# Kernel tuning notes

Measured on AMD Instinct MI355X. Metric: run time of the kernel, lower is better.

Reference implementation:

```python
import jax, jax.numpy as jnp
import numpy as np

ROT = 0.7071  # matches the literal used in DiagPool's affine theta
EPS = 1e-5    # GroupNorm default eps


def conv2d(x, w, pad):
    # x: (N,C,H,W), w: (O,I,kh,kw)
    return jax.lax.conv_general_dilated(
        x, w, window_strides=(1, 1), padding=[(pad, pad), (pad, pad)],
        dimension_numbers=("NCHW", "OIHW", "NCHW"))


def diag_pool(x):
    """Replicates F.affine_grid + F.grid_sample (align_corners=False, bilinear,
    zeros padding) with a 45-degree rotation, then mean over H (keepdim)."""
    N, C, H, W = x.shape
    dt = x.dtype
    xn = ((2.0 * jnp.arange(W, dtype=dt) + 1.0) / W - 1.0)  # normalized x coords
    yn = ((2.0 * jnp.arange(H, dtype=dt) + 1.0) / H - 1.0)  # normalized y coords
    Yn, Xn = jnp.meshgrid(yn, xn, indexing="ij")            # (H,W)
    xs = ROT * Xn - ROT * Yn   # theta row 0
    ys = ROT * Xn + ROT * Yn   # theta row 1
    # unnormalize (align_corners=False)
    xp = ((xs + 1.0) * W - 1.0) * 0.5
    yp = ((ys + 1.0) * H - 1.0) * 0.5
    x0 = jnp.floor(xp); y0 = jnp.floor(yp)
    x1 = x0 + 1.0;      y1 = y0 + 1.0
    wx1 = xp - x0; wx0 = 1.0 - wx1
    wy1 = yp - y0; wy0 = 1.0 - wy1

    def gather(yi, xi):
        valid = ((yi >= 0) & (yi < H) & (xi >= 0) & (xi < W)).astype(dt)
        yc = jnp.clip(yi, 0, H - 1).astype(jnp.int32)
        xc = jnp.clip(xi, 0, W - 1).astype(jnp.int32)
        return x[:, :, yc, xc] * valid  # (N,C,H,W)

    rot = (gather(y0, x0) * (wy0 * wx0) + gather(y0, x1) * (wy0 * wx1)
           + gather(y1, x0) * (wy1 * wx0) + gather(y1, x1) * (wy1 * wx1))
    return rot.mean(axis=2, keepdims=True)  # (N,C,1,W)


def group_norm_per_channel(x, g, b):
    # GroupNorm(cg, cg): each channel normalized over its own (H,W)
    mu = x.mean(axis=(2, 3), keepdims=True)
    var = x.var(axis=(2, 3), keepdims=True)
    xh = (x - mu) * jax.lax.rsqrt(var + EPS)
    return xh * g[None, :, None, None] + b[None, :, None, None]


def cross_axis_encode(gx, axis_fuse_w, gn_w, gn_b):
    N, cg, H, W = gx.shape
    x_h = gx.mean(axis=3, keepdims=True)                 # (N,cg,H,1)
    x_w = gx.mean(axis=2, keepdims=True)                 # (N,cg,1,W)
    x_d = diag_pool(gx)                                  # (N,cg,1,W)
    fused = jnp.concatenate(
        [x_h, x_w.transpose(0, 1, 3, 2), x_d.transpose(0, 1, 3, 2)], axis=2)  # (N,cg,H+2W,1)
    fused = conv2d(fused, axis_fuse_w, 0)
    x_h2 = fused[:, :, :H]          # (N,cg,H,1)
    x_w2 = fused[:, :, H:H + W]     # (N,cg,W,1)
    out = gx * jax.nn.sigmoid(x_h2) * jax.nn.sigmoid(x_w2.transpose(0, 1, 3, 2))
    return group_norm_per_channel(out, gn_w, gn_b)


def setup_inputs() -> dict:
    key = jax.random.key(0)
    B, C, H, W = 8, 256, 128, 128
    G = 32
    cg = C // G  # 8
    ks = jax.random.split(key, 10)
    s = 0.1
    return {
        "x": jax.random.normal(ks[0], (B, C, H, W), jnp.float32),
        "axis_fuse_w": jax.random.normal(ks[1], (cg, cg, 1, 1), jnp.float32) * s,
        "gn_w": jnp.ones((cg,), jnp.float32),
        "gn_b": jnp.zeros((cg,), jnp.float32),
        "conv1x1_w": jax.random.normal(ks[2], (cg, cg, 1, 1), jnp.float32) * s,
        "conv3x3_w": jax.random.normal(ks[3], (cg, cg, 3, 3), jnp.float32) * s,
        "conv5x5_w": jax.random.normal(ks[4], (cg, cg, 5, 5), jnp.float32) * s,
        "scale_w": jnp.ones((3,), jnp.float32),
        "ch_gate_w": jax.random.normal(ks[5], (cg, cg, 1, 1), jnp.float32) * s,
        "sp_gate_w": jax.random.normal(ks[6], (1, cg, 1, 1), jnp.float32) * s,
        "groups": 32,
    }


def reference(x, axis_fuse_w, gn_w, gn_b, conv1x1_w, conv3x3_w, conv5x5_w,
              scale_w, ch_gate_w, sp_gate_w, groups):
    B, C, H, W = x.shape
    cg = C // groups
    N = B * groups
    gx = x.reshape(N, cg, H, W)

    xa = cross_axis_encode(gx, axis_fuse_w, gn_w, gn_b)
    xa = conv2d(xa, conv1x1_w, 0)
    xb = conv2d(gx, conv3x3_w, 1)
    xc = conv2d(gx, conv5x5_w, 2)

    sw = jax.nn.softmax(scale_w)
    x1 = sw[0] * xa + sw[1] * xb + sw[2] * xc
    x2 = xb

    def ch_gate(t):
        return jax.nn.sigmoid(conv2d(t.mean(axis=(2, 3), keepdims=True), ch_gate_w, 0))

    def sp_gate(t):
        return jax.nn.sigmoid(conv2d(t, sp_gate_w, 0))

    x1 = x1 * ch_gate(x1) * sp_gate(x1)
    x2 = x2 * ch_gate(x2) * sp_gate(x2)

    x11 = jax.nn.softmax(x1.mean(axis=(2, 3)).reshape(N, 1, cg), axis=-1)  # (N,1,cg)
    x12 = x2.reshape(N, cg, H * W)
    x21 = jax.nn.softmax(x2.mean(axis=(2, 3)).reshape(N, 1, cg), axis=-1)
    x22 = x1.reshape(N, cg, H * W)
    weights = (x11 @ x12 + x21 @ x22).reshape(N, 1, H, W)
    return (gx * jax.nn.sigmoid(weights)).reshape(B, C, H, W)
```

## Files before the change

kernel.cpp:

```cpp
#include <hip/hip_runtime.h>
#include <math.h>

#define HH 128
#define WW 128
#define CG 8
#define NN 256
#define HWSZ (HH*WW)
#define GB (36*36*8)

typedef __bf16 bf16x8 __attribute__((ext_vector_type(8)));
typedef short short8v __attribute__((ext_vector_type(8)));
typedef float f32x4 __attribute__((ext_vector_type(4)));

__device__ __forceinline__ float sigmoidf_(float x){ return 1.0f/(1.0f+__expf(-x)); }

__device__ __forceinline__ unsigned short f2bf(float x){
  __bf16 h = (__bf16)x;
  return __builtin_bit_cast(unsigned short, h);
}
__device__ __forceinline__ float bf2f(unsigned short h){
  union { unsigned u; float f; } v; v.u = ((unsigned)h) << 16; return v.f;
}

__device__ __forceinline__ float wx1_(const float* w1, const float* w3, const float* w5,
                                      float sw0, float sw1, float sw2,
                                      int oc, int ic, int tap){
  if (tap < 25){
    int ky = tap/5, kx = tap - ky*5;
    float wv = sw2 * w5[oc*200 + ic*25 + tap];
    if (ky >= 1 && ky <= 3 && kx >= 1 && kx <= 3)
      wv = fmaf(sw1, w3[oc*72 + ic*9 + (ky-1)*3 + (kx-1)], wv);
    return wv;
  }
  if (tap == 25) return sw0 * w1[oc*CG + ic];
  return 0.f;
}
__device__ __forceinline__ float wx2_(const float* w3, int oc, int ic, int tap){
  if (tap < 25){
    int ky = tap/5, kx = tap - ky*5;
    if (ky >= 1 && ky <= 3 && kx >= 1 && kx <= 3)
      return w3[oc*72 + ic*9 + (ky-1)*3 + (kx-1)];
  }
  return 0.f;
}

__global__ void kWB(const float* __restrict__ w1, const float* __restrict__ w3,
                    const float* __restrict__ w5, const float* __restrict__ scw,
                    const float* __restrict__ spw,
                    unsigned short* __restrict__ BH, unsigned short* __restrict__ BL){
  int e = blockIdx.x*256 + threadIdx.x;
  float a = scw[0], b = scw[1], c = scw[2];
  float m = fmaxf(a, fmaxf(b, c));
  float e0 = __expf(a-m), e1 = __expf(b-m), e2 = __expf(c-m);
  float inv = 1.0f/(e0+e1+e2);
  float sw0 = e0*inv, sw1 = e1*inv, sw2 = e2*inv;
  if (e < 3584){
    int s = e >> 9, rem = e & 511, nn = rem >> 5, kk = rem & 31;
    int tap = s*4 + (kk >> 3), ic = kk & 7;
    float wv = (nn < 8) ? wx1_(w1,w3,w5,sw0,sw1,sw2,nn,ic,tap)
                        : wx2_(w3,nn-8,ic,tap);
    BH[e] = f2bf(wv);
  } else if (e < 5824){
    int e2 = e - 3584;
    int s = e2 / 320, rem = e2 - s*320, nn = rem >> 5, kk = rem & 31;
    int tap = s*4 + (kk >> 3), ic = kk & 7;
    float outv;
    if (nn < 8){
      float wv = wx1_(w1,w3,w5,sw0,sw1,sw2,nn,ic,tap);
      outv = wv - bf2f(f2bf(wv));
    } else {
      float sum = 0.f;
      #pragma unroll
      for (int oc = 0; oc < CG; ++oc){
        float wv = (nn == 8) ? wx1_(w1,w3,w5,sw0,sw1,sw2,oc,ic,tap)
                             : wx2_(w3,oc,ic,tap);
        sum = fmaf(spw[oc], wv, sum);
      }
      outv = sum;
    }
    BL[e2] = f2bf(outv);
  }
}

__global__ __launch_bounds__(256) void kA1(const float* __restrict__ gx,
                                           float* __restrict__ xh_ws,
                                           float* __restrict__ xw_ws){
  int b = blockIdx.x; int n = b >> 3; int c = b & 7;
  int tid = threadIdx.x;
  __shared__ float colpart[2][WW];
  const float* img = gx + (size_t)(n*CG+c)*HWSZ;
  int w = tid & 127, half = tid >> 7;
  float acc = 0.f;
  const float* p = img + half*64*WW + w;
  for (int h = 0; h < 64; ++h) acc += p[h*WW];
  colpart[half][w] = acc;
  int h2 = tid >> 1, wh = tid & 1;
  float racc = 0.f;
  const float* rp = img + h2*WW + wh*64;
  for (int j = 0; j < 64; ++j) racc += rp[j];
  racc += __shfl_xor(racc, 1);
  __syncthreads();
  if (tid < WW) xw_ws[(n*CG+c)*WW + tid] = (colpart[0][tid] + colpart[1][tid]) * (1.0f/HH);
  if (wh == 0) xh_ws[(n*CG+c)*HH + h2] = racc * (1.0f/WW);
}

__global__ __launch_bounds__(256) void kA2(const float* __restrict__ xh_ws,
                                           const float* __restrict__ xw_ws,
                                           const float* __restrict__ afw,
                                           float* __restrict__ sig_h,
                                           float* __restrict__ sig_w){
  int n = blockIdx.x;
  int tid = threadIdx.x;
  if (tid < HH){
    int h = tid;
    float v[CG];
    #pragma unroll
    for (int c = 0; c < CG; ++c) v[c] = xh_ws[(n*CG+c)*HH + h];
    #pragma unroll
    for (int o = 0; o < CG; ++o){
      float s = 0.f;
      #pragma unroll
      for (int i = 0; i < CG; ++i) s = fmaf(afw[o*CG+i], v[i], s);
      sig_h[(n*CG+o)*HH + h] = sigmoidf_(s);
    }
  } else {
    int w = tid - 128;
    float v[CG];
    #pragma unroll
    for (int c = 0; c < CG; ++c) v[c] = xw_ws[(n*CG+c)*WW + w];
    #pragma unroll
    for (int o = 0; o < CG; ++o){
      float s = 0.f;
      #pragma unroll
      for (int i = 0; i < CG; ++i) s = fmaf(afw[o*CG+i], v[i], s);
      sig_w[(n*CG+o)*WW + w] = sigmoidf_(s);
    }
  }
}

__global__ __launch_bounds__(256) void kB(const float* __restrict__ gx,
                                          const float* __restrict__ sig_h,
                                          const float* __restrict__ sig_w,
                                          const float* __restrict__ gn_w,
                                          const float* __restrict__ gn_b,
                                          float* __restrict__ Bgn,
                                          float* __restrict__ sighA){
  int b = blockIdx.x; int n = b >> 3; int c = b & 7;
  int tid = threadIdx.x;
  __shared__ float sh[HH];
  __shared__ float swv[WW];
  __shared__ float red[16];
  __shared__ float sAb;
  if (tid < HH) sh[tid] = sig_h[(n*CG+c)*HH + tid];
  else          swv[tid-128] = sig_w[(n*CG+c)*WW + tid - 128];
  __syncthreads();
  const float* img = gx + (size_t)(n*CG+c)*HWSZ;
  float s1 = 0.f, s2 = 0.f;
  for (int idx = tid; idx < HWSZ; idx += 256){
    int h = idx >> 7, w = idx & 127;
    float t = img[idx] * sh[h] * swv[w];
    s1 += t; s2 = fmaf(t, t, s2);
  }
  #pragma unroll
  for (int off = 32; off; off >>= 1){ s1 += __shfl_down(s1, off); s2 += __shfl_down(s2, off); }
  int wv = tid >> 6, ln = tid & 63;
  if (ln == 0){ red[wv] = s1; red[8+wv] = s2; }
  __syncthreads();
  if (tid == 0){
    float S1 = red[0]+red[1]+red[2]+red[3];
    float S2 = red[8]+red[9]+red[10]+red[11];
    float mu  = S1 * (1.0f/HWSZ);
    float var = S2 * (1.0f/HWSZ) - mu*mu;
    float rstd = rsqrtf(var + 1e-5f);
    float A = rstd * gn_w[c];
    Bgn[n*CG+c] = gn_b[c] - mu*A;
    sAb = A;
  }
  __syncthreads();
  if (tid < HH) sighA[(n*CG+c)*HH + tid] = sh[tid] * sAb;
}

__global__ __launch_bounds__(256) void kC(const float* __restrict__ gx,
                                          const float* __restrict__ w1,
                                          const float* __restrict__ scale_w,
                                          const float* __restrict__ spw,
                                          const float* __restrict__ sig_w,
                                          const float* __restrict__ sighA,
                                          const float* __restrict__ Bgn,
                                          const unsigned short* __restrict__ BHg,
                                          const unsigned short* __restrict__ BLog,
                                          unsigned short* __restrict__ x1m,
                                          unsigned short* __restrict__ x2m,
                                          float* __restrict__ gacc){
  __shared__ __align__(16) unsigned short tile[36*36*8 + 32*32*8];
  __shared__ float shf[CG*32];
  __shared__ float swf[CG*32];
  __shared__ float constA[CG];

  int tid = threadIdx.x;
  int bb = blockIdx.x;
  int n  = bb >> 4;
  int t_ = bb & 15;
  int y0 = (t_ >> 2) * 32;
  int x0 = (t_ & 3) * 32;

  int lane = tid & 63, wid = tid >> 6;
  int pr = lane & 15, tg = lane >> 4;

  bf16x8 bH[7], bL[7];
  #pragma unroll
  for (int s = 0; s < 7; ++s)
    bH[s] = *reinterpret_cast<const bf16x8*>(BHg + s*512 + pr*32 + tg*8);
  short8v zs = {0,0,0,0,0,0,0,0};
  bf16x8 zb = __builtin_bit_cast(bf16x8, zs);
  if (pr < 10){
    #pragma unroll
    for (int s = 0; s < 7; ++s)
      bL[s] = *reinterpret_cast<const bf16x8*>(BLog + s*320 + pr*32 + tg*8);
  } else {
    #pragma unroll
    for (int s = 0; s < 7; ++s) bL[s] = zb;
  }

  float sw0;
  {
    float a = scale_w[0], b = scale_w[1], c = scale_w[2];
    float m = fmaxf(a, fmaxf(b, c));
    float e0 = __expf(a-m), e1 = __expf(b-m), e2 = __expf(c-m);
    sw0 = e0 / (e0+e1+e2);
  }
  {
    int ic = tid >> 5, k = tid & 31;
    shf[ic*32+k] = sighA[(n*CG+ic)*HH + y0 + k];
    swf[ic*32+k] = sig_w[(n*CG+ic)*WW + x0 + k];
  }
  if (tid < CG){
    float s = 0.f;
    #pragma unroll
    for (int i = 0; i < CG; ++i) s = fmaf(w1[tid*CG+i], Bgn[n*CG+i], s);
    constA[tid] = sw0 * s;
  }
  __syncthreads();

  const float* base_n = gx + (size_t)n*CG*HWSZ;
  for (int e = tid; e < 1296; e += 256){
    int yy = e / 36, xx = e - yy*36;
    int gy = y0 + yy - 2, gz = x0 + xx - 2;
    float v[8];
    uint4 pk; unsigned* pw = (unsigned*)&pk;
    if ((unsigned)gy < HH && (unsigned)gz < WW){
      int o = gy*WW + gz;
      #pragma unroll
      for (int p = 0; p < 4; ++p){
        v[2*p]   = base_n[(size_t)(2*p)*HWSZ + o];
        v[2*p+1] = base_n[(size_t)(2*p+1)*HWSZ + o];
        pw[p] = (unsigned)f2bf(v[2*p]) | ((unsigned)f2bf(v[2*p+1]) << 16);
      }
    } else {
      #pragma unroll
      for (int p = 0; p < 4; ++p){ v[2*p] = 0.f; v[2*p+1] = 0.f; pw[p] = 0u; }
    }
    *reinterpret_cast<uint4*>(&tile[e*8]) = pk;
    int yl = yy - 2, xl = xx - 2;
    if ((unsigned)yl < 32u && (unsigned)xl < 32u){
      uint4 gk; unsigned* gw = (unsigned*)&gk;
      #pragma unroll
      for (int p = 0; p < 4; ++p){
        float t0 = v[2*p]   * shf[(2*p)*32   + yl] * swf[(2*p)*32   + xl];
        float t1 = v[2*p+1] * shf[(2*p+1)*32 + yl] * swf[(2*p+1)*32 + xl];
        gw[p] = (unsigned)f2bf(t0) | ((unsigned)f2bf(t1) << 16);
      }
      *reinterpret_cast<uint4*>(&tile[GB + (yl*32 + xl)*8]) = gk;
    }
  }

  int strd[7], ofs[7];
  #pragma unroll
  for (int s = 0; s < 7; ++s){
    int t = s*4 + tg;
    if (t < 25){ int ky = t/5, kx = t - ky*5; strd[s] = 36*8; ofs[s] = (ky*36 + kx)*8; }
    else if (t == 25){ strd[s] = 32*8; ofs[s] = GB; }
    else { strd[s] = 36*8; ofs[s] = 0; }
  }
  float Cd1 = 0.f;
  #pragma unroll
  for (int oc = 0; oc < CG; ++oc) Cd1 = fmaf(spw[oc], constA[oc], Cd1);
  float cA = (pr < 8) ? constA[pr] : 0.f;
  int gsrc = (lane & 48) | (pr < 8 ? 8 : 9);
  __syncthreads();

  float sAcc = 0.f, qAcc = 0.f;

#define EPI(P, Q, GXX) do { \
    float gq[4]; \
    _Pragma("unroll") \
    for (int r = 0; r < 4; ++r) gq[r] = __shfl(Q[r], gsrc); \
    ushort4 u; \
    _Pragma("unroll") \
    for (int r = 0; r < 4; ++r){ \
      float vvr = (pr < 8) ? (P[r] + Q[r] + cA) : P[r]; \
      float d   = (pr < 8) ? (gq[r] + Cd1) : gq[r]; \
      float sg  = sigmoidf_(d); \
      sAcc += vvr; \
      qAcc = fmaf(vvr, sg, qAcc); \
      ((unsigned short*)&u)[r] = f2bf(vvr); \
    } \
    size_t off = ((size_t)(n*CG + (pr & 7))*HH + (y0 + yl))*WW + (GXX); \
    if (pr < 8) *reinterpret_cast<ushort4*>(x1m + off) = u; \
    else        *reinterpret_cast<ushort4*>(x2m + off) = u; \
  } while(0)

  #pragma unroll 1
  for (int ii = 0; ii < 8; ++ii){
    int yl = wid*8 + ii;
    f32x4 P0 = {0.f,0.f,0.f,0.f}, Q0 = {0.f,0.f,0.f,0.f};
    f32x4 P1 = {0.f,0.f,0.f,0.f}, Q1 = {0.f,0.f,0.f,0.f};
    #pragma unroll
    for (int s = 0; s < 7; ++s){
      const unsigned short* ap = &tile[yl*strd[s] + ofs[s] + pr*8];
      bf16x8 a0 = *reinterpret_cast<const bf16x8*>(ap);
      bf16x8 a1 = *reinterpret_cast<const bf16x8*>(ap + 128);
      P0 = __builtin_amdgcn_mfma_f32_16x16x32_bf16(a0, bH[s], P0, 0, 0, 0);
      Q0 = __builtin_amdgcn_mfma_f32_16x16x32_bf16(a0, bL[s], Q0, 0, 0, 0);
      P1 = __builtin_amdgcn_mfma_f32_16x16x32_bf16(a1, bH[s], P1, 0, 0, 0);
      Q1 = __builtin_amdgcn_mfma_f32_16x16x32_bf16(a1, bL[s], Q1, 0, 0, 0);
    }
    EPI(P0, Q0, x0 + tg*4);
    EPI(P1, Q1, x0 + 16 + tg*4);
  }
#undef EPI

  sAcc += __shfl_xor(sAcc, 16); sAcc += __shfl_xor(sAcc, 32);
  qAcc += __shfl_xor(qAcc, 16); qAcc += __shfl_xor(qAcc, 32);
  if (lane < 16){
    int b0 = (pr < 8) ? pr : (8 + pr);
    atomicAdd(&gacc[n*32 + b0],     sAcc);
    atomicAdd(&gacc[n*32 + b0 + 8], qAcc);
  }
}

__global__ void kT(const float* __restrict__ gacc, const float* __restrict__ cgw,
                   float* __restrict__ a1a2){
  int n = blockIdx.x*blockDim.x + threadIdx.x;
  if (n >= NN) return;
  const float* g = gacc + n*32;
  float m1[CG], q1[CG], m2[CG], q2[CG];
  #pragma unroll
  for (int c = 0; c < CG; ++c){
    m1[c] = g[c]      * (1.0f/HWSZ);
    q1[c] = g[8+c]    * (1.0f/HWSZ);
    m2[c] = g[16+c]   * (1.0f/HWSZ);
    q2[c] = g[24+c]   * (1.0f/HWSZ);
  }
  float chg1[CG], chg2[CG];
  #pragma unroll
  for (int o = 0; o < CG; ++o){
    float s1 = 0.f, s2 = 0.f;
    #pragma unroll
    for (int i = 0; i < CG; ++i){ s1 = fmaf(cgw[o*CG+i], m1[i], s1); s2 = fmaf(cgw[o*CG+i], m2[i], s2); }
    chg1[o] = sigmoidf_(s1); chg2[o] = sigmoidf_(s2);
  }
  float z1[CG], z2[CG];
  float mx1 = -1e30f, mx2 = -1e30f;
  #pragma unroll
  for (int c = 0; c < CG; ++c){
    z1[c] = chg1[c]*q1[c]; z2[c] = chg2[c]*q2[c];
    mx1 = fmaxf(mx1, z1[c]); mx2 = fmaxf(mx2, z2[c]);
  }
  float su1 = 0.f, su2 = 0.f;
  #pragma unroll
  for (int c = 0; c < CG; ++c){
    z1[c] = __expf(z1[c]-mx1); su1 += z1[c];
    z2[c] = __expf(z2[c]-mx2); su2 += z2[c];
  }
  float i1 = 1.0f/su1, i2 = 1.0f/su2;
  #pragma unroll
  for (int c = 0; c < CG; ++c){
    float x11 = z1[c]*i1;
    float x21 = z2[c]*i2;
    a1a2[n*16 + c]     = x21 * chg1[c];
    a1a2[n*16 + 8 + c] = x11 * chg2[c];
  }
}

__global__ __launch_bounds__(256) void kF(const float* __restrict__ gx,
                                          const unsigned short* __restrict__ x1m,
                                          const unsigned short* __restrict__ x2m,
                                          const float* __restrict__ a1a2,
                                          const float* __restrict__ spw,
                                          float* __restrict__ out){
  int tid = threadIdx.x;
  int bb = blockIdx.x;
  int n  = bb >> 4;
  int hw = ((bb & 15) << 10) + tid*4;
  size_t base = (size_t)(n*CG)*HWSZ + hw;
  float a1[CG], a2[CG], sp[CG];
  #pragma unroll
  for (int c = 0; c < CG; ++c){
    a1[c] = a1a2[n*16 + c];
    a2[c] = a1a2[n*16 + 8 + c];
    sp[c] = spw[c];
  }
  float d1[4]  = {0.f,0.f,0.f,0.f}, dd1[4] = {0.f,0.f,0.f,0.f};
  float d2[4]  = {0.f,0.f,0.f,0.f}, dd2[4] = {0.f,0.f,0.f,0.f};
  #pragma unroll
  for (int c = 0; c < CG; ++c){
    ushort4 u1 = *reinterpret_cast<const ushort4*>(x1m + base + (size_t)c*HWSZ);
    ushort4 u2 = *reinterpret_cast<const ushort4*>(x2m + base + (size_t)c*HWSZ);
    #pragma unroll
    for (int p = 0; p < 4; ++p){
      float v1 = bf2f(((const unsigned short*)&u1)[p]);
      float v2 = bf2f(((const unsigned short*)&u2)[p]);
      d1[p]  = fmaf(sp[c], v1, d1[p]);  dd1[p] = fmaf(a1[c], v1, dd1[p]);
      d2[p]  = fmaf(sp[c], v2, d2[p]);  dd2[p] = fmaf(a2[c], v2, dd2[p]);
    }
  }
  float sW[4];
  #pragma unroll
  for (int p = 0; p < 4; ++p){
    float Wv = sigmoidf_(d1[p])*dd1[p] + sigmoidf_(d2[p])*dd2[p];
    sW[p] = sigmoidf_(Wv);
  }
  #pragma unroll
  for (int c = 0; c < CG; ++c){
    float4 g = *reinterpret_cast<const float4*>(gx + base + (size_t)c*HWSZ);
    float4 o;
    o.x = g.x*sW[0]; o.y = g.y*sW[1]; o.z = g.z*sW[2]; o.w = g.w*sW[3];
    *reinterpret_cast<float4*>(out + base + (size_t)c*HWSZ) = o;
  }
}

extern "C" void kernel_launch(void* const* d_in, const int* in_sizes, int n_in,
                              void* d_out, int out_size, void* d_ws, size_t ws_size,
                              hipStream_t stream){
  const float* x   = (const float*)d_in[0];
  const float* afw = (const float*)d_in[1];
  const float* gnw = (const float*)d_in[2];
  const float* gnb = (const float*)d_in[3];
  const float* w1  = (const float*)d_in[4];
  const float* w3  = (const float*)d_in[5];
  const float* w5  = (const float*)d_in[6];
  const float* scw = (const float*)d_in[7];
  const float* cgw = (const float*)d_in[8];
  const float* spw = (const float*)d_in[9];

  char* ws = (char*)d_ws;
  float* sig_h = (float*)(ws + 0);
  float* sig_w = (float*)(ws + 1048576);
  unsigned short* BHg  = (unsigned short*)(ws + 2097152);
  float* a1a2 = (float*)(ws + 2097152);
  unsigned short* BLog = (unsigned short*)(ws + 2113536);
  unsigned short* x1m = (unsigned short*)(ws + 2121728);
  unsigned short* x2m = (unsigned short*)(ws + 2121728 + 67108864);

  float* out = (float*)d_out;
  float* xh_ws = (float*)d_out;
  float* xw_ws = (float*)d_out + 262144;
  float* sighA = (float*)((char*)d_out + 2097152);
  float* Bgn   = (float*)((char*)d_out + 3145728);
  float* gacc  = (float*)((char*)d_out + 3153920);

  hipMemsetAsync(gacc, 0, NN*32*sizeof(float), stream);
  kWB<<<23, 256, 0, stream>>>(w1, w3, w5, scw, spw, BHg, BLog);
  kA1<<<NN*CG, 256, 0, stream>>>(x, xh_ws, xw_ws);
  kA2<<<NN, 256, 0, stream>>>(xh_ws, xw_ws, afw, sig_h, sig_w);
  kB <<<NN*CG, 256, 0, stream>>>(x, sig_h, sig_w, gnw, gnb, Bgn, sighA);
  kC <<<NN*16, 256, 0, stream>>>(x, w1, scw, spw, sig_w, sighA, Bgn, BHg, BLog, x1m, x2m, gacc);
  kT <<<4, 64, 0, stream>>>(gacc, cgw, a1a2);
  kF <<<NN*16, 256, 0, stream>>>(x, x1m, x2m, a1a2, spw, out);
}
```

Measured before the change: 447.1 us.

## Emit channel-interleaved bf16 copy of input in kB and read it in kC

kB now handles all 8 channels of a group per block, computing the GroupNorm statistics with float4 loads. While it has the data in registers it writes a channel-interleaved bf16 copy of the input into scratch space in the output buffer. kC then loads one 16-byte vector per pixel from this packed copy instead of eight strided fp32 loads plus conversion, which cuts its halo-tile global traffic. The separate memset is folded into an extra block of kWB. The cost is an extra write pass of the bf16 tensor, and kB now launches 8x fewer blocks, which could lower memory-level parallelism.

```diff
diff --git a/kernel.cpp b/kernel.cpp
--- a/kernel.cpp
+++ b/kernel.cpp
@@ -47,7 +47,12 @@
 __global__ void kWB(const float* __restrict__ w1, const float* __restrict__ w3,
                     const float* __restrict__ w5, const float* __restrict__ scw,
                     const float* __restrict__ spw,
-                    unsigned short* __restrict__ BH, unsigned short* __restrict__ BL){
+                    unsigned short* __restrict__ BH, unsigned short* __restrict__ BL,
+                    float* __restrict__ gacc){
+  if (blockIdx.x == 23){
+    for (int i = threadIdx.x; i < NN*32; i += 256) gacc[i] = 0.f;
+    return;
+  }
   int e = blockIdx.x*256 + threadIdx.x;
   float a = scw[0], b = scw[1], c = scw[2];
   float m = fmaxf(a, fmaxf(b, c));
@@ -144,43 +149,82 @@
                                           const float* __restrict__ gn_w,
                                           const float* __restrict__ gn_b,
                                           float* __restrict__ Bgn,
-                                          float* __restrict__ sighA){
-  int b = blockIdx.x; int n = b >> 3; int c = b & 7;
+                                          float* __restrict__ sighA,
+                                          unsigned short* __restrict__ xbf){
+  int n = blockIdx.x;
   int tid = threadIdx.x;
-  __shared__ float sh[HH];
-  __shared__ float swv[WW];
-  __shared__ float red[16];
-  __shared__ float sAb;
-  if (tid < HH) sh[tid] = sig_h[(n*CG+c)*HH + tid];
-  else          swv[tid-128] = sig_w[(n*CG+c)*WW + tid - 128];
+  __shared__ float sh[CG][HH];
+  __shared__ float swv[CG][WW];
+  __shared__ float red[2][CG][4];
+  __shared__ float sA[CG];
+  for (int i = tid; i < CG*HH; i += 256) sh[i>>7][i&127] = sig_h[n*CG*HH + i];
+  for (int i = tid; i < CG*WW; i += 256) swv[i>>7][i&127] = sig_w[n*CG*WW + i];
   __syncthreads();
-  const float* img = gx + (size_t)(n*CG+c)*HWSZ;
-  float s1 = 0.f, s2 = 0.f;
-  for (int idx = tid; idx < HWSZ; idx += 256){
-    int h = idx >> 7, w = idx & 127;
-    float t = img[idx] * sh[h] * swv[w];
-    s1 += t; s2 = fmaf(t, t, s2);
-  }
-  #pragma unroll
-  for (int off = 32; off; off >>= 1){ s1 += __shfl_down(s1, off); s2 += __shfl_down(s2, off); }
+  const float* base = gx + (size_t)n*CG*HWSZ;
+  unsigned short* xb = xbf + (size_t)n*HWSZ*8;
+  float s1[CG], s2[CG];
+  #pragma unroll
+  for (int c = 0; c < CG; ++c){ s1[c] = 0.f; s2[c] = 0.f; }
+  for (int it = 0; it < 16; ++it){
+    int px = (it*256 + tid)*4;
+    int h = px >> 7, w = px & 127;
+    float4 v[CG];
+    #pragma unroll
+    for (int c = 0; c < CG; ++c)
+      v[c] = *reinterpret_cast<const float4*>(base + (size_t)c*HWSZ + px);
+    #pragma unroll
+    for (int c = 0; c < CG; ++c){
+      float shc = sh[c][h];
+      const float* vc = (const float*)&v[c];
+      #pragma unroll
+      for (int j = 0; j < 4; ++j){
+        float t = vc[j] * shc * swv[c][w+j];
+        s1[c] += t; s2[c] = fmaf(t, t, s2[c]);
+      }
+    }
+    #pragma unroll
+    for (int j = 0; j < 4; ++j){
+      uint4 pk; unsigned* pw = (unsigned*)&pk;
+      #pragma unroll
+      for (int p = 0; p < 4; ++p){
+        float a0 = ((const float*)&v[2*p])[j];
+        float a1 = ((const float*)&v[2*p+1])[j];
+        pw[p] = (unsigned)f2bf(a0) | ((unsigned)f2bf(a1) << 16);
+      }
+      *reinterpret_cast<uint4*>(xb + (size_t)(px + j)*8) = pk;
+    }
+  }
   int wv = tid >> 6, ln = tid & 63;
-  if (ln == 0){ red[wv] = s1; red[8+wv] = s2; }
+  #pragma unroll
+  for (int c = 0; c < CG; ++c){
+    #pragma unroll
+    for (int off = 32; off; off >>= 1){
+      s1[c] += __shfl_down(s1[c], off);
+      s2[c] += __shfl_down(s2[c], off);
+    }
+  }
+  if (ln == 0){
+    #pragma unroll
+    for (int c = 0; c < CG; ++c){ red[0][c][wv] = s1[c]; red[1][c][wv] = s2[c]; }
+  }
   __syncthreads();
-  if (tid == 0){
-    float S1 = red[0]+red[1]+red[2]+red[3];
-    float S2 = red[8]+red[9]+red[10]+red[11];
+  if (tid < CG){
+    int c = tid;
+    float S1 = red[0][c][0]+red[0][c][1]+red[0][c][2]+red[0][c][3];
+    float S2 = red[1][c][0]+red[1][c][1]+red[1][c][2]+red[1][c][3];
     float mu  = S1 * (1.0f/HWSZ);
     float var = S2 * (1.0f/HWSZ) - mu*mu;
     float rstd = rsqrtf(var + 1e-5f);
     float A = rstd * gn_w[c];
     Bgn[n*CG+c] = gn_b[c] - mu*A;
-    sAb = A;
+    sA[c] = A;
   }
   __syncthreads();
-  if (tid < HH) sighA[(n*CG+c)*HH + tid] = sh[tid] * sAb;
-}
-
-__global__ __launch_bounds__(256) void kC(const float* __restrict__ gx,
+  for (int i = tid; i < CG*HH; i += 256)
+    sighA[n*CG*HH + i] = sh[i>>7][i&127] * sA[i>>7];
+}
+
+__global__ __launch_bounds__(256) void kC(const unsigned short* __restrict__ xbf,
                                           const float* __restrict__ w1,
                                           const float* __restrict__ scale_w,
                                           const float* __restrict__ spw,
@@ -242,32 +286,26 @@
   }
   __syncthreads();
 
-  const float* base_n = gx + (size_t)n*CG*HWSZ;
+  const unsigned short* xb = xbf + (size_t)n*HWSZ*8;
   for (int e = tid; e < 1296; e += 256){
     int yy = e / 36, xx = e - yy*36;
     int gy = y0 + yy - 2, gz = x0 + xx - 2;
-    float v[8];
-    uint4 pk; unsigned* pw = (unsigned*)&pk;
-    if ((unsigned)gy < HH && (unsigned)gz < WW){
-      int o = gy*WW + gz;
-      #pragma unroll
-      for (int p = 0; p < 4; ++p){
-        v[2*p]   = base_n[(size_t)(2*p)*HWSZ + o];
-        v[2*p+1] = base_n[(size_t)(2*p+1)*HWSZ + o];
-        pw[p] = (unsigned)f2bf(v[2*p]) | ((unsigned)f2bf(v[2*p+1]) << 16);
-      }
-    } else {
-      #pragma unroll
-      for (int p = 0; p < 4; ++p){ v[2*p] = 0.f; v[2*p+1] = 0.f; pw[p] = 0u; }
-    }
+    uint4 pk;
+    if ((unsigned)gy < HH && (unsigned)gz < WW)
+      pk = *reinterpret_cast<const uint4*>(xb + (size_t)(gy*WW + gz)*8);
+    else
+      pk = make_uint4(0u, 0u, 0u, 0u);
     *reinterpret_cast<uint4*>(&tile[e*8]) = pk;
     int yl = yy - 2, xl = xx - 2;
     if ((unsigned)yl < 32u && (unsigned)xl < 32u){
+      unsigned* pw = (unsigned*)&pk;
       uint4 gk; unsigned* gw = (unsigned*)&gk;
       #pragma unroll
       for (int p = 0; p < 4; ++p){
-        float t0 = v[2*p]   * shf[(2*p)*32   + yl] * swf[(2*p)*32   + xl];
-        float t1 = v[2*p+1] * shf[(2*p+1)*32 + yl] * swf[(2*p+1)*32 + xl];
+        float lo = __builtin_bit_cast(float, pw[p] << 16);
+        float hi = __builtin_bit_cast(float, pw[p] & 0xffff0000u);
+        float t0 = lo * shf[(2*p)*32   + yl] * swf[(2*p)*32   + xl];
+        float t1 = hi * shf[(2*p+1)*32 + yl] * swf[(2*p+1)*32 + xl];
         gw[p] = (unsigned)f2bf(t0) | ((unsigned)f2bf(t1) << 16);
       }
       *reinterpret_cast<uint4*>(&tile[GB + (yl*32 + xl)*8]) = gk;
@@ -459,13 +497,13 @@
   float* sighA = (float*)((char*)d_out + 2097152);
   float* Bgn   = (float*)((char*)d_out + 3145728);
   float* gacc  = (float*)((char*)d_out + 3153920);
-
-  hipMemsetAsync(gacc, 0, NN*32*sizeof(float), stream);
-  kWB<<<23, 256, 0, stream>>>(w1, w3, w5, scw, spw, BHg, BLog);
+  unsigned short* xbf = (unsigned short*)((char*)d_out + 4194304);
+
+  kWB<<<24, 256, 0, stream>>>(w1, w3, w5, scw, spw, BHg, BLog, gacc);
   kA1<<<NN*CG, 256, 0, stream>>>(x, xh_ws, xw_ws);
   kA2<<<NN, 256, 0, stream>>>(xh_ws, xw_ws, afw, sig_h, sig_w);
-  kB <<<NN*CG, 256, 0, stream>>>(x, sig_h, sig_w, gnw, gnb, Bgn, sighA);
-  kC <<<NN*16, 256, 0, stream>>>(x, w1, scw, spw, sig_w, sighA, Bgn, BHg, BLog, x1m, x2m, gacc);
+  kB <<<NN, 256, 0, stream>>>(x, sig_h, sig_w, gnw, gnb, Bgn, sighA, xbf);
+  kC <<<NN*16, 256, 0, stream>>>(xbf, w1, scw, spw, sig_w, sighA, Bgn, BHg, BLog, x1m, x2m, gacc);
   kT <<<4, 64, 0, stream>>>(gacc, cgw, a1a2);
   kF <<<NN*16, 256, 0, stream>>>(x, x1m, x2m, a1a2, spw, out);
 }
```

Result: no change. 449.4 us (+0.5%).
